# Optimization experiments

Measured on AMD Instinct MI355X. Metric: run time of the kernel, lower is better.

Reference implementation:

```python
import jax, jax.numpy as jnp
import numpy as np

SMALL_NUMBER = 1e-07
N, C, H, D = 100000, 128, 128, 3  # nodes, input_size, hidden_size, spatial dim


def _glorot(key, shape):
    r = np.sqrt(6.0 / (shape[-2] + shape[-1]))
    return jax.random.uniform(key, shape, dtype=jnp.float32, minval=-r, maxval=r)


def setup_inputs() -> dict:
    key = jax.random.key(0)
    ks = jax.random.split(key, 12)
    return {
        "v": jax.random.normal(ks[0], (N, C, D), dtype=jnp.float32),
        "m_v": jax.random.normal(ks[1], (N, H, D), dtype=jnp.float32),
        "Wh_z": _glorot(ks[2], (H, C)),
        "Wi_z": _glorot(ks[3], (C, C)),
        "b_z": jnp.zeros((1, C), dtype=jnp.float32),
        "Wh_r": _glorot(ks[4], (H, C)),
        "Wi_r": _glorot(ks[5], (C, C)),
        "b_r": jnp.zeros((1, C), dtype=jnp.float32),
        "Wh_v": _glorot(ks[6], (H, C)),
        "Wi_v": _glorot(ks[7], (C, C)),
        "Wq": _glorot(ks[8], (C, C)),
        "Wk": _glorot(ks[9], (C, C)),
    }


def _vlin(x, w):
    # x: [N, C_in, D], w: [C_in, C_out] -> [N, C_out, D]
    return jnp.einsum('ncd,co->nod', x, w)


def _vn_leaky(x, Wq, Wk, alpha=0.3):
    # x: [N, C, D]
    Q = jnp.einsum('ncd,cq->nqd', x, Wq)  # [N, C, D]
    K = jnp.einsum('ncd,ck->nkd', x, Wk)  # [N, C, D]
    inner = jnp.einsum('ncd,ncd->nc', Q, K)           # [N, C]
    inner = jnp.minimum(inner, 0.0)[:, :, None]        # inner * (inner < 0)
    k_norm = jnp.linalg.norm(K, axis=-1)[:, :, None] + SMALL_NUMBER  # [N, C, 1]
    out = Q - inner * K / jnp.square(k_norm)
    return alpha * x + (1.0 - alpha) * out


def reference(v, m_v, Wh_z, Wi_z, b_z, Wh_r, Wi_r, b_r, Wh_v, Wi_v, Wq, Wk):
    z = _vlin(m_v, Wh_z) + _vlin(v, Wi_z)                       # [N, C, D]
    z = jax.nn.sigmoid(jnp.linalg.norm(z, axis=-1) + b_z)[:, :, None]  # [N, C, 1]
    r = _vlin(m_v, Wh_r) + _vlin(v, Wi_r)
    r = jax.nn.sigmoid(jnp.linalg.norm(r, axis=-1) + b_r)[:, :, None]
    delta_v = _vlin(m_v, Wh_v) + _vlin(r * v, Wi_v)
    delta_v = _vn_leaky(delta_v, Wq, Wk)
    return (1.0 - z) * v + z * delta_v
```

## Files before the change

### kernel.cpp

```cpp
#include <hip/hip_runtime.h>


#define NN   100000
#define NT   16
#define NBLK (NN / NT)
#define PSZ  16384

typedef unsigned short us;
typedef us     us8    __attribute__((ext_vector_type(8)));
typedef __bf16 bf16x8 __attribute__((ext_vector_type(8)));
typedef float  f32x4  __attribute__((ext_vector_type(4)));

#define MFMA __builtin_amdgcn_mfma_f32_16x16x32_bf16

__device__ __forceinline__ us f2b(float f) {
    union { float f; unsigned u; } x; x.f = f;
    return (us)((x.u + 0x7FFFu + ((x.u >> 16) & 1u)) >> 16);
}
__device__ __forceinline__ float b2f(us h) {
    union { unsigned u; float f; } x; x.u = ((unsigned)h) << 16;
    return x.f;
}

__device__ __forceinline__ int aoff(int d, int i, int c) {
    return ((d * 4 + (c >> 5)) * 64 + (i + (((c >> 3) & 3) << 4))) * 8 + (c & 7);
}

__global__ void prep_weights(const float* __restrict__ Whz, const float* __restrict__ Wiz,
                             const float* __restrict__ Whr, const float* __restrict__ Wir,
                             const float* __restrict__ Whv, const float* __restrict__ Wiv,
                             const float* __restrict__ Wq,  const float* __restrict__ Wk,
                             us* __restrict__ ws) {
    const int mid = blockIdx.x >> 3;
    const int s = ((blockIdx.x & 7) << 8) + threadIdx.x;
    const float* W; int hp, lp;
    switch (mid) {
        case 0: W = Whz; hp = 0;  lp = -1; break;
        case 1: W = Wiz; hp = 1;  lp = -1; break;
        case 2: W = Whr; hp = 2;  lp = 3;  break;
        case 3: W = Wir; hp = 4;  lp = 5;  break;
        case 4: W = Whv; hp = 6;  lp = 7;  break;
        case 5: W = Wiv; hp = 8;  lp = 9;  break;
        case 6: W = Wq;  hp = 10; lp = -1; break;
        default: W = Wk; hp = 11; lp = 12; break;
    }
    const int f = s >> 6, l = s & 63;
    const int o  = (f >> 2) * 16 + (l & 15);
    const int c0 = (f & 3) * 32 + (l >> 4) * 8;
    us8 hi, lo;
#pragma unroll
    for (int j = 0; j < 8; ++j) {
        float x = W[(c0 + j) * 128 + o];
        us h = f2b(x);
        hi[j] = h;
        lo[j] = f2b(x - b2f(h));
    }
    *(us8*)(ws + hp * PSZ + s * 8) = hi;
    if (lp >= 0) *(us8*)(ws + lp * PSZ + s * 8) = lo;
}

__device__ __forceinline__ void mm_zr(const us* __restrict__ Ah, const us* __restrict__ Al,
                                      const us* __restrict__ pz, const us* __restrict__ prh,
                                      const us* __restrict__ prl,
                                      f32x4* zacc, f32x4* racc, int wb, int ab) {
#pragma unroll
    for (int kf = 0; kf < 4; ++kf) {
        bf16x8 bz = *(const bf16x8*)(pz  + wb + kf * 512);
        bf16x8 bh = *(const bf16x8*)(prh + wb + kf * 512);
        bf16x8 bl = *(const bf16x8*)(prl + wb + kf * 512);
#pragma unroll
        for (int m = 0; m < 3; ++m) {
            bf16x8 ah = *(const bf16x8*)(Ah + (m * 4 + kf) * 512 + ab);
            bf16x8 al = *(const bf16x8*)(Al + (m * 4 + kf) * 512 + ab);
            zacc[m] = MFMA(ah, bz, zacc[m], 0, 0, 0);
            racc[m] = MFMA(ah, bh, racc[m], 0, 0, 0);
            racc[m] = MFMA(al, bh, racc[m], 0, 0, 0);
            racc[m] = MFMA(ah, bl, racc[m], 0, 0, 0);
        }
    }
}
__device__ __forceinline__ void mm_s(const us* __restrict__ Ah, const us* __restrict__ Al,
                                     const us* __restrict__ ph, const us* __restrict__ pl,
                                     f32x4* acc, int wb, int ab) {
#pragma unroll
    for (int kf = 0; kf < 4; ++kf) {
        bf16x8 bh = *(const bf16x8*)(ph + wb + kf * 512);
        bf16x8 bl = *(const bf16x8*)(pl + wb + kf * 512);
#pragma unroll
        for (int m = 0; m < 3; ++m) {
            bf16x8 ah = *(const bf16x8*)(Ah + (m * 4 + kf) * 512 + ab);
            bf16x8 al = *(const bf16x8*)(Al + (m * 4 + kf) * 512 + ab);
            acc[m] = MFMA(ah, bh, acc[m], 0, 0, 0);
            acc[m] = MFMA(al, bh, acc[m], 0, 0, 0);
            acc[m] = MFMA(ah, bl, acc[m], 0, 0, 0);
        }
    }
}
__device__ __forceinline__ void mm_qk(const us* __restrict__ Dh, const us* __restrict__ Dl,
                                      const us* __restrict__ pq, const us* __restrict__ pkh,
                                      const us* __restrict__ pkl,
                                      f32x4* qacc, f32x4* kacc, int wb, int ab) {
#pragma unroll
    for (int kf = 0; kf < 4; ++kf) {
        bf16x8 bq = *(const bf16x8*)(pq  + wb + kf * 512);
        bf16x8 bh = *(const bf16x8*)(pkh + wb + kf * 512);
        bf16x8 bl = *(const bf16x8*)(pkl + wb + kf * 512);
#pragma unroll
        for (int m = 0; m < 3; ++m) {
            bf16x8 dh = *(const bf16x8*)(Dh + (m * 4 + kf) * 512 + ab);
            bf16x8 dl = *(const bf16x8*)(Dl + (m * 4 + kf) * 512 + ab);
            qacc[m] = MFMA(dh, bq, qacc[m], 0, 0, 0);
            kacc[m] = MFMA(dh, bh, kacc[m], 0, 0, 0);
            kacc[m] = MFMA(dl, bh, kacc[m], 0, 0, 0);
            kacc[m] = MFMA(dh, bl, kacc[m], 0, 0, 0);
        }
    }
}

__global__ __launch_bounds__(512, 4) void gru_vn_fused(
    const float* __restrict__ v, const float* __restrict__ mv,
    const float* __restrict__ bz, const float* __restrict__ br,
    const us* __restrict__ ws, float* __restrict__ out)
{
    __shared__ __align__(16) us mvh[6144], mvl[6144];
    __shared__ __align__(16) us vth[6144], vtl[6144];
    __shared__ __align__(16) float r_t[2048];

    const int tid  = threadIdx.x;
    const int lane = tid & 63;
    const int wave = tid >> 6;
    const int arow = lane & 15;
    const int bo   = wave * 16 + arow;
    const int rsub = (lane >> 4) * 4;
    const int ab   = lane * 8;
    const int wb   = wave * 2048 + lane * 8;
    const int n0   = blockIdx.x * NT;

    const us* pWhz  = ws;            const us* pWiz  = ws + 1 * PSZ;
    const us* pWhrh = ws + 2 * PSZ;  const us* pWhrl = ws + 3 * PSZ;
    const us* pWirh = ws + 4 * PSZ;  const us* pWirl = ws + 5 * PSZ;
    const us* pWhvh = ws + 6 * PSZ;  const us* pWhvl = ws + 7 * PSZ;
    const us* pWivh = ws + 8 * PSZ;  const us* pWivl = ws + 9 * PSZ;
    const us* pWq   = ws + 10 * PSZ; const us* pWkh  = ws + 11 * PSZ;
    const us* pWkl  = ws + 12 * PSZ;

    {
        const float* vs = v  + (size_t)n0 * 384;
        const float* ms = mv + (size_t)n0 * 384;
#pragma unroll
        for (int it = 0; it < 3; ++it) {
            int base = tid * 4 + it * 2048;
            float4 a = *(const float4*)(vs + base);
            float4 b = *(const float4*)(ms + base);
            const float* ap = &a.x; const float* bp = &b.x;
#pragma unroll
            for (int j = 0; j < 4; ++j) {
                int idx = base + j;
                int i = idx / 384, rem = idx - i * 384;
                int c = rem / 3, d = rem - c * 3;
                int off = aoff(d, i, c);
                float av = ap[j], bv = bp[j];
                us h;
                h = f2b(av); vth[off] = h; vtl[off] = f2b(av - b2f(h));
                h = f2b(bv); mvh[off] = h; mvl[off] = f2b(bv - b2f(h));
            }
        }
    }
    const float bzv = bz[bo], brv = br[bo];
    const f32x4 Z4 = {0.f, 0.f, 0.f, 0.f};
    __syncthreads();

    f32x4 zacc[3] = {Z4, Z4, Z4}, racc[3] = {Z4, Z4, Z4};
    mm_zr(mvh, mvl, pWhz, pWhrh, pWhrl, zacc, racc, wb, ab);
    mm_zr(vth, vtl, pWiz, pWirh, pWirl, zacc, racc, wb, ab);

    float zz[4], vout[4][3];
#pragma unroll
    for (int q = 0; q < 4; ++q) {
        float h0 = zacc[0][q], h1 = zacc[1][q], h2 = zacc[2][q];
        zz[q] = 1.f / (1.f + __expf(-(sqrtf(h0 * h0 + h1 * h1 + h2 * h2) + bzv)));
        float r0 = racc[0][q], r1 = racc[1][q], r2 = racc[2][q];
        float rr = 1.f / (1.f + __expf(-(sqrtf(r0 * r0 + r1 * r1 + r2 * r2) + brv)));
        r_t[(rsub + q) * 128 + bo] = rr;
#pragma unroll
        for (int d = 0; d < 3; ++d) {
            int off = aoff(d, rsub + q, bo);
            vout[q][d] = b2f(vth[off]) + b2f(vtl[off]);
        }
    }
    __syncthreads();

#pragma unroll
    for (int it = 0; it < 2; ++it) {
        int s = tid + it * 512;
        if (s < 768) {
            int f = s >> 6, l = s & 63;
            int i = l & 15, c0 = (f & 3) * 32 + (l >> 4) * 8;
            us8 vh = *(const us8*)(vth + s * 8);
            us8 vl = *(const us8*)(vtl + s * 8);
            us8 oh, ol;
#pragma unroll
            for (int j = 0; j < 8; ++j) {
                float p = r_t[i * 128 + c0 + j] * (b2f(vh[j]) + b2f(vl[j]));
                us h = f2b(p);
                oh[j] = h; ol[j] = f2b(p - b2f(h));
            }
            *(us8*)(vth + s * 8) = oh;
            *(us8*)(vtl + s * 8) = ol;
        }
    }
    __syncthreads();

    f32x4 dacc[3] = {Z4, Z4, Z4};
    mm_s(mvh, mvl, pWhvh, pWhvl, dacc, wb, ab);
    mm_s(vth, vtl, pWivh, pWivl, dacc, wb, ab);
    __syncthreads();

#pragma unroll
    for (int m = 0; m < 3; ++m)
#pragma unroll
    for (int q = 0; q < 4; ++q) {
        int off = aoff(m, rsub + q, bo);
        float x = dacc[m][q];
        us h = f2b(x);
        mvh[off] = h;
        mvl[off] = f2b(x - b2f(h));
    }
    __syncthreads();

    f32x4 qacc[3] = {Z4, Z4, Z4}, kacc[3] = {Z4, Z4, Z4};
    mm_qk(mvh, mvl, pWq, pWkh, pWkl, qacc, kacc, wb, ab);

#pragma unroll
    for (int q = 0; q < 4; ++q) {
        const int i = rsub + q;
        float q0 = qacc[0][q], q1 = qacc[1][q], q2 = qacc[2][q];
        float k0 = kacc[0][q], k1 = kacc[1][q], k2 = kacc[2][q];
        float inner = fminf(q0 * k0 + q1 * k1 + q2 * k2, 0.f);
        float kn = sqrtf(k0 * k0 + k1 * k1 + k2 * k2) + 1e-7f;
        float s = inner / (kn * kn);
        float z = zz[q];
        float dv0 = 0.3f * dacc[0][q] + 0.7f * (q0 - s * k0);
        float dv1 = 0.3f * dacc[1][q] + 0.7f * (q1 - s * k1);
        float dv2 = 0.3f * dacc[2][q] + 0.7f * (q2 - s * k2);
        float* op = out + ((size_t)(n0 + i) * 128 + bo) * 3;
        op[0] = (1.f - z) * vout[q][0] + z * dv0;
        op[1] = (1.f - z) * vout[q][1] + z * dv1;
        op[2] = (1.f - z) * vout[q][2] + z * dv2;
    }
}

extern "C" void kernel_launch(void* const* d_in, const int* in_sizes, int n_in,
                              void* d_out, int out_size, void* d_ws, size_t ws_size,
                              hipStream_t stream) {
    (void)in_sizes; (void)n_in; (void)ws_size; (void)out_size;
    us* ws = (us*)d_ws;
    prep_weights<<<64, 256, 0, stream>>>(
        (const float*)d_in[2],  (const float*)d_in[3],
        (const float*)d_in[5],  (const float*)d_in[6],
        (const float*)d_in[8],  (const float*)d_in[9],
        (const float*)d_in[10], (const float*)d_in[11], ws);
    gru_vn_fused<<<NBLK, 512, 0, stream>>>(
        (const float*)d_in[0], (const float*)d_in[1],
        (const float*)d_in[4], (const float*)d_in[7],
        ws, (float*)d_out);
}
```

Measured before the change: 264.7 us.

## Vectorize input staging, prefetch weight fragments before barriers, pad r_t layout

The input load now has each thread read 12 contiguous floats of one node and write packed us4 bf16 hi/lo values per spatial dimension into LDS. This replaces scalar scattered stores that needed divisions. Weight B fragments are loaded into registers before each __syncthreads so the global/L2 latency overlaps the barrier and the LDS work. r_t is transposed with a stride-17 pad to avoid LDS bank conflicts, and the bf16 conversion uses the native __bf16 cast. Holding the prefetched fragments raises register pressure, which may hurt occupancy under launch_bounds(512,4).

```diff
diff --git a/kernel.cpp b/kernel.cpp
--- a/kernel.cpp
+++ b/kernel.cpp
@@ -7,6 +7,7 @@
 #define PSZ  16384
 
 typedef unsigned short us;
+typedef us     us4    __attribute__((ext_vector_type(4)));
 typedef us     us8    __attribute__((ext_vector_type(8)));
 typedef __bf16 bf16x8 __attribute__((ext_vector_type(8)));
 typedef float  f32x4  __attribute__((ext_vector_type(4)));
@@ -20,10 +21,6 @@
 __device__ __forceinline__ float b2f(us h) {
     union { unsigned u; float f; } x; x.u = ((unsigned)h) << 16;
     return x.f;
-}
-
-__device__ __forceinline__ int aoff(int d, int i, int c) {
-    return ((d * 4 + (c >> 5)) * 64 + (i + (((c >> 3) & 3) << 4))) * 8 + (c & 7);
 }
 
 __global__ void prep_weights(const float* __restrict__ Whz, const float* __restrict__ Wiz,
@@ -59,62 +56,54 @@
     if (lp >= 0) *(us8*)(ws + lp * PSZ + s * 8) = lo;
 }
 
+__device__ __forceinline__ void loadB4(const us* __restrict__ p, int wb, bf16x8* d) {
+#pragma unroll
+    for (int kf = 0; kf < 4; ++kf) d[kf] = *(const bf16x8*)(p + wb + kf * 512);
+}
+
 __device__ __forceinline__ void mm_zr(const us* __restrict__ Ah, const us* __restrict__ Al,
-                                      const us* __restrict__ pz, const us* __restrict__ prh,
-                                      const us* __restrict__ prl,
-                                      f32x4* zacc, f32x4* racc, int wb, int ab) {
-#pragma unroll
-    for (int kf = 0; kf < 4; ++kf) {
-        bf16x8 bz = *(const bf16x8*)(pz  + wb + kf * 512);
-        bf16x8 bh = *(const bf16x8*)(prh + wb + kf * 512);
-        bf16x8 bl = *(const bf16x8*)(prl + wb + kf * 512);
+                                      const bf16x8* bz, const bf16x8* bh, const bf16x8* bl,
+                                      f32x4* zacc, f32x4* racc, int ab) {
+#pragma unroll
+    for (int kf = 0; kf < 4; ++kf)
 #pragma unroll
         for (int m = 0; m < 3; ++m) {
             bf16x8 ah = *(const bf16x8*)(Ah + (m * 4 + kf) * 512 + ab);
             bf16x8 al = *(const bf16x8*)(Al + (m * 4 + kf) * 512 + ab);
-            zacc[m] = MFMA(ah, bz, zacc[m], 0, 0, 0);
-            racc[m] = MFMA(ah, bh, racc[m], 0, 0, 0);
-            racc[m] = MFMA(al, bh, racc[m], 0, 0, 0);
-            racc[m] = MFMA(ah, bl, racc[m], 0, 0, 0);
-        }
-    }
+            zacc[m] = MFMA(ah, bz[kf], zacc[m], 0, 0, 0);
+            racc[m] = MFMA(ah, bh[kf], racc[m], 0, 0, 0);
+            racc[m] = MFMA(al, bh[kf], racc[m], 0, 0, 0);
+            racc[m] = MFMA(ah, bl[kf], racc[m], 0, 0, 0);
+        }
 }
 __device__ __forceinline__ void mm_s(const us* __restrict__ Ah, const us* __restrict__ Al,
-                                     const us* __restrict__ ph, const us* __restrict__ pl,
-                                     f32x4* acc, int wb, int ab) {
-#pragma unroll
-    for (int kf = 0; kf < 4; ++kf) {
-        bf16x8 bh = *(const bf16x8*)(ph + wb + kf * 512);
-        bf16x8 bl = *(const bf16x8*)(pl + wb + kf * 512);
+                                     const bf16x8* bh, const bf16x8* bl,
+                                     f32x4* acc, int ab) {
+#pragma unroll
+    for (int kf = 0; kf < 4; ++kf)
 #pragma unroll
         for (int m = 0; m < 3; ++m) {
             bf16x8 ah = *(const bf16x8*)(Ah + (m * 4 + kf) * 512 + ab);
             bf16x8 al = *(const bf16x8*)(Al + (m * 4 + kf) * 512 + ab);
-            acc[m] = MFMA(ah, bh, acc[m], 0, 0, 0);
-            acc[m] = MFMA(al, bh, acc[m], 0, 0, 0);
-            acc[m] = MFMA(ah, bl, acc[m], 0, 0, 0);
-        }
-    }
+            acc[m] = MFMA(ah, bh[kf], acc[m], 0, 0, 0);
+            acc[m] = MFMA(al, bh[kf], acc[m], 0, 0, 0);
+            acc[m] = MFMA(ah, bl[kf], acc[m], 0, 0, 0);
+        }
 }
 __device__ __forceinline__ void mm_qk(const us* __restrict__ Dh, const us* __restrict__ Dl,
-                                      const us* __restrict__ pq, const us* __restrict__ pkh,
-                                      const us* __restrict__ pkl,
-                                      f32x4* qacc, f32x4* kacc, int wb, int ab) {
-#pragma unroll
-    for (int kf = 0; kf < 4; ++kf) {
-        bf16x8 bq = *(const bf16x8*)(pq  + wb + kf * 512);
-        bf16x8 bh = *(const bf16x8*)(pkh + wb + kf * 512);
-        bf16x8 bl = *(const bf16x8*)(pkl + wb + kf * 512);
+                                      const bf16x8* bq, const bf16x8* bh, const bf16x8* bl,
+                                      f32x4* qacc, f32x4* kacc, int ab) {
+#pragma unroll
+    for (int kf = 0; kf < 4; ++kf)
 #pragma unroll
         for (int m = 0; m < 3; ++m) {
             bf16x8 dh = *(const bf16x8*)(Dh + (m * 4 + kf) * 512 + ab);
             bf16x8 dl = *(const bf16x8*)(Dl + (m * 4 + kf) * 512 + ab);
-            qacc[m] = MFMA(dh, bq, qacc[m], 0, 0, 0);
-            kacc[m] = MFMA(dh, bh, kacc[m], 0, 0, 0);
-            kacc[m] = MFMA(dl, bh, kacc[m], 0, 0, 0);
-            kacc[m] = MFMA(dh, bl, kacc[m], 0, 0, 0);
-        }
-    }
+            qacc[m] = MFMA(dh, bq[kf], qacc[m], 0, 0, 0);
+            kacc[m] = MFMA(dh, bh[kf], kacc[m], 0, 0, 0);
+            kacc[m] = MFMA(dl, bh[kf], kacc[m], 0, 0, 0);
+            kacc[m] = MFMA(dh, bl[kf], kacc[m], 0, 0, 0);
+        }
 }
 
 __global__ __launch_bounds__(512, 4) void gru_vn_fused(
@@ -124,7 +113,7 @@
 {
     __shared__ __align__(16) us mvh[6144], mvl[6144];
     __shared__ __align__(16) us vth[6144], vtl[6144];
-    __shared__ __align__(16) float r_t[2048];
+    __shared__ __align__(16) float r_t[128 * 17];
 
     const int tid  = threadIdx.x;
     const int lane = tid & 63;
@@ -145,35 +134,52 @@
     const us* pWkl  = ws + 12 * PSZ;
 
     {
-        const float* vs = v  + (size_t)n0 * 384;
-        const float* ms = mv + (size_t)n0 * 384;
-#pragma unroll
-        for (int it = 0; it < 3; ++it) {
-            int base = tid * 4 + it * 2048;
-            float4 a = *(const float4*)(vs + base);
-            float4 b = *(const float4*)(ms + base);
-            const float* ap = &a.x; const float* bp = &b.x;
-#pragma unroll
-            for (int j = 0; j < 4; ++j) {
-                int idx = base + j;
-                int i = idx / 384, rem = idx - i * 384;
-                int c = rem / 3, d = rem - c * 3;
-                int off = aoff(d, i, c);
-                float av = ap[j], bv = bp[j];
-                us h;
-                h = f2b(av); vth[off] = h; vtl[off] = f2b(av - b2f(h));
-                h = f2b(bv); mvh[off] = h; mvl[off] = f2b(bv - b2f(h));
+        const int ind = tid >> 5;
+        const int q4  = tid & 31;
+        const int c0s = q4 * 4;
+        const float* vp = v  + (size_t)(n0 + ind) * 384 + q4 * 12;
+        const float* mp = mv + (size_t)(n0 + ind) * 384 + q4 * 12;
+        float xv[12], xm[12];
+        *(float4*)(xv + 0) = *(const float4*)(vp + 0);
+        *(float4*)(xv + 4) = *(const float4*)(vp + 4);
+        *(float4*)(xv + 8) = *(const float4*)(vp + 8);
+        *(float4*)(xm + 0) = *(const float4*)(mp + 0);
+        *(float4*)(xm + 4) = *(const float4*)(mp + 4);
+        *(float4*)(xm + 8) = *(const float4*)(mp + 8);
+        const int sb = ((c0s >> 5) * 64 + ind + (((c0s >> 3) & 3) << 4)) * 8 + (c0s & 7);
+#pragma unroll
+        for (int d = 0; d < 3; ++d) {
+            us4 vh4, vl4, mh4, ml4;
+#pragma unroll
+            for (int e = 0; e < 4; ++e) {
+                float x = xv[d + e * 3];
+                __bf16 h = (__bf16)x;
+                vh4[e] = __builtin_bit_cast(us, h);
+                vl4[e] = __builtin_bit_cast(us, (__bf16)(x - (float)h));
+                x = xm[d + e * 3];
+                h = (__bf16)x;
+                mh4[e] = __builtin_bit_cast(us, h);
+                ml4[e] = __builtin_bit_cast(us, (__bf16)(x - (float)h));
             }
+            *(us4*)(vth + sb + d * 2048) = vh4;
+            *(us4*)(vtl + sb + d * 2048) = vl4;
+            *(us4*)(mvh + sb + d * 2048) = mh4;
+            *(us4*)(mvl + sb + d * 2048) = ml4;
         }
     }
     const float bzv = bz[bo], brv = br[bo];
     const f32x4 Z4 = {0.f, 0.f, 0.f, 0.f};
+
+    bf16x8 Bz[4], Brh[4], Brl[4];
+    loadB4(pWhz, wb, Bz); loadB4(pWhrh, wb, Brh); loadB4(pWhrl, wb, Brl);
     __syncthreads();
 
     f32x4 zacc[3] = {Z4, Z4, Z4}, racc[3] = {Z4, Z4, Z4};
-    mm_zr(mvh, mvl, pWhz, pWhrh, pWhrl, zacc, racc, wb, ab);
-    mm_zr(vth, vtl, pWiz, pWirh, pWirl, zacc, racc, wb, ab);
-
+    mm_zr(mvh, mvl, Bz, Brh, Brl, zacc, racc, ab);
+    loadB4(pWiz, wb, Bz); loadB4(pWirh, wb, Brh); loadB4(pWirl, wb, Brl);
+    mm_zr(vth, vtl, Bz, Brh, Brl, zacc, racc, ab);
+
+    const int vbase = ((bo >> 5) * 64 + rsub + (((bo >> 3) & 3) << 4)) * 8 + (bo & 7);
     float zz[4], vout[4][3];
 #pragma unroll
     for (int q = 0; q < 4; ++q) {
@@ -181,13 +187,15 @@
         zz[q] = 1.f / (1.f + __expf(-(sqrtf(h0 * h0 + h1 * h1 + h2 * h2) + bzv)));
         float r0 = racc[0][q], r1 = racc[1][q], r2 = racc[2][q];
         float rr = 1.f / (1.f + __expf(-(sqrtf(r0 * r0 + r1 * r1 + r2 * r2) + brv)));
-        r_t[(rsub + q) * 128 + bo] = rr;
+        r_t[bo * 17 + rsub + q] = rr;
 #pragma unroll
         for (int d = 0; d < 3; ++d) {
-            int off = aoff(d, rsub + q, bo);
+            int off = vbase + d * 2048 + q * 8;
             vout[q][d] = b2f(vth[off]) + b2f(vtl[off]);
         }
     }
+    bf16x8 Bdh[4], Bdl[4];
+    loadB4(pWhvh, wb, Bdh); loadB4(pWhvl, wb, Bdl);
     __syncthreads();
 
 #pragma unroll
@@ -195,15 +203,16 @@
         int s = tid + it * 512;
         if (s < 768) {
             int f = s >> 6, l = s & 63;
-            int i = l & 15, c0 = (f & 3) * 32 + (l >> 4) * 8;
-            us8 vh = *(const us8*)(vth + s * 8);
-            us8 vl = *(const us8*)(vtl + s * 8);
+            int i = l & 15, cb = (f & 3) * 32 + (l >> 4) * 8;
+            us8 vh8 = *(const us8*)(vth + s * 8);
+            us8 vl8 = *(const us8*)(vtl + s * 8);
             us8 oh, ol;
 #pragma unroll
             for (int j = 0; j < 8; ++j) {
-                float p = r_t[i * 128 + c0 + j] * (b2f(vh[j]) + b2f(vl[j]));
-                us h = f2b(p);
-                oh[j] = h; ol[j] = f2b(p - b2f(h));
+                float p = r_t[(cb + j) * 17 + i] * (b2f(vh8[j]) + b2f(vl8[j]));
+                __bf16 h = (__bf16)p;
+                oh[j] = __builtin_bit_cast(us, h);
+                ol[j] = __builtin_bit_cast(us, (__bf16)(p - (float)h));
             }
             *(us8*)(vth + s * 8) = oh;
             *(us8*)(vtl + s * 8) = ol;
@@ -212,24 +221,27 @@
     __syncthreads();
 
     f32x4 dacc[3] = {Z4, Z4, Z4};
-    mm_s(mvh, mvl, pWhvh, pWhvl, dacc, wb, ab);
-    mm_s(vth, vtl, pWivh, pWivl, dacc, wb, ab);
+    mm_s(mvh, mvl, Bdh, Bdl, dacc, ab);
+    loadB4(pWivh, wb, Bdh); loadB4(pWivl, wb, Bdl);
+    mm_s(vth, vtl, Bdh, Bdl, dacc, ab);
     __syncthreads();
 
 #pragma unroll
     for (int m = 0; m < 3; ++m)
 #pragma unroll
     for (int q = 0; q < 4; ++q) {
-        int off = aoff(m, rsub + q, bo);
+        int off = vbase + m * 2048 + q * 8;
         float x = dacc[m][q];
-        us h = f2b(x);
-        mvh[off] = h;
-        mvl[off] = f2b(x - b2f(h));
-    }
+        __bf16 h = (__bf16)x;
+        mvh[off] = __builtin_bit_cast(us, h);
+        mvl[off] = __builtin_bit_cast(us, (__bf16)(x - (float)h));
+    }
+    bf16x8 Bq[4], Bkh[4], Bkl[4];
+    loadB4(pWq, wb, Bq); loadB4(pWkh, wb, Bkh); loadB4(pWkl, wb, Bkl);
     __syncthreads();
 
     f32x4 qacc[3] = {Z4, Z4, Z4}, kacc[3] = {Z4, Z4, Z4};
-    mm_qk(mvh, mvl, pWq, pWkh, pWkl, qacc, kacc, wb, ab);
+    mm_qk(mvh, mvl, Bq, Bkh, Bkl, qacc, kacc, ab);
 
 #pragma unroll
     for (int q = 0; q < 4; ++q) {
```

Result: faster. 237.9 us (-10.1%).
